# Performance work log

Measured on AMD Instinct MI355X. Metric: run time of the kernel, lower is better.

The kernel has to match this reference:

```python
import jax, jax.numpy as jnp
import numpy as np

NUM_CLASSES = 10
LAMBDA_UNCERTAINTY = 0.5
IGNORE_INDEX = 10
B, H, W = 8, 512, 512


def setup_inputs() -> dict:
    key = jax.random.key(0)
    k1, k2 = jax.random.split(key)
    logits = jax.random.normal(k1, (B, NUM_CLASSES, H, W), dtype=jnp.float32)
    targets = jax.random.randint(k2, (B, H, W), 0, 11)  # includes ignore_index=10
    return {"logits": logits, "targets": targets}


def reference(logits, targets):
    C = NUM_CLASSES
    f32 = logits.dtype

    # entropy of the predicted distribution (torch adds 1e-8 inside log)
    probs = jax.nn.softmax(logits, axis=1)                      # [B,C,H,W]
    log_probs = jnp.log(probs + 1e-8)
    entropy = -jnp.sum(probs * log_probs, axis=1)               # [B,H,W]

    valid = targets != IGNORE_INDEX                             # [B,H,W] bool
    valid_f = valid.astype(f32)
    n_valid = jnp.sum(valid_f)                                  # scalar

    # single-pass scatter-mean replacing the per-class python loop
    t_clip = jnp.clip(targets, 0, C - 1)
    t_flat = t_clip.reshape(-1)
    v_flat = valid_f.reshape(-1)
    counts = jax.ops.segment_sum(v_flat, t_flat, num_segments=C)                    # n_c per class
    ent_sum = jax.ops.segment_sum(entropy.reshape(-1) * v_flat, t_flat, num_segments=C)

    has_samples = (counts > 0) & (n_valid > 0)
    w_base = jnp.where(has_samples, (n_valid - counts) / jnp.maximum(n_valid, 1.0), 0.0)
    entropy_mean = jnp.where(counts > 0, ent_sum / jnp.maximum(counts, 1.0), 0.0)
    w_combined = w_base * (1.0 + LAMBDA_UNCERTAINTY * entropy_mean)                 # [C]

    weight_map = w_combined[t_clip] * valid_f                   # [B,H,W]

    # per-pixel cross entropy, zeroed at ignore_index (torch F.cross_entropy semantics)
    log_sm = jax.nn.log_softmax(logits, axis=1)                 # [B,C,H,W]
    ce = -jnp.take_along_axis(log_sm, t_clip[:, None], axis=1)[:, 0]  # [B,H,W]
    ce = ce * valid_f

    return jnp.sum(ce * weight_map) / (n_valid + 1e-6)
```

## Files before the change

kernel.cpp:

```cpp
#include <hip/hip_runtime.h>

#define NCLS 10
#define IGN 10
#define HW_ (512 * 512)
#define BATCH 8
#define NPIX (BATCH * HW_)
#define THREADS 256
#define PPT 2
#define CHUNK_PX (THREADS * PPT)
#define CHUNKS 4
#define BLOCK_PX (CHUNK_PX * CHUNKS)
#define NBLOCKS (NPIX / BLOCK_PX)
#define STAT_STRIDE 16
#define LAMBDA_UNC 0.5f
#define LOG2E 1.4426950408889634f
#define LN2 0.6931471805599453f

#define RSTRIDE 33
#define HISTSZ (THREADS * RSTRIDE)

typedef const __attribute__((address_space(1))) void GV;
typedef __attribute__((address_space(3))) void LV;
__device__ __forceinline__ void gload_lds16(const void* g, void* l) {
    __builtin_amdgcn_global_load_lds((GV*)g, (LV*)l, 16, 0, 0);
}

__global__ void awce_zero_stats(float* __restrict__ stats) {
    int i = threadIdx.x;
    if (i < 30 * STAT_STRIDE) stats[i] = 0.0f;
}

template <bool ATOMIC>
__global__ __launch_bounds__(THREADS) void awce_main(
    const float* __restrict__ logits,
    const int* __restrict__ targets,
    float* __restrict__ outbuf)
{
    const int tid = threadIdx.x;
    const int wave = tid >> 6;
    const int lane = tid & 63;

    __shared__ float stage[2][11][CHUNK_PX];
    __shared__ float hist[HISTSZ];
    __shared__ float red[4][32];

    const int g0 = blockIdx.x * BLOCK_PX;
    const int b = g0 >> 18;
    const int hw0 = g0 & (HW_ - 1);
    const float* lbase = logits + (size_t)b * (NCLS * (size_t)HW_);

    auto stage_chunk = [&](int k, int s) {
#pragma unroll
        for (int i = wave; i < 22; i += 4) {
            const int c = i >> 1;
            const int h = i & 1;
            const int pxo = h * 256 + (lane << 2);
            const void* gsrc;
            if (c < 10)
                gsrc = (const void*)(lbase + (size_t)c * HW_ + hw0 + k * CHUNK_PX + pxo);
            else
                gsrc = (const void*)(targets + g0 + k * CHUNK_PX + pxo);
            gload_lds16(gsrc, (void*)&stage[s][c][h * 256]);
        }
    };

    stage_chunk(0, 0);
#pragma unroll
    for (int i = 0; i < RSTRIDE; ++i) hist[tid + i * THREADS] = 0.0f;
    __syncthreads();

    float* hreg = &hist[tid * RSTRIDE];

#pragma unroll
    for (int k = 0; k < CHUNKS; ++k) {
        const int s = k & 1;
        float x[NCLS][PPT];
#pragma unroll
        for (int c = 0; c < NCLS; ++c) {
            float2 v = *reinterpret_cast<float2*>(&stage[s][c][tid * PPT]);
            x[c][0] = v.x; x[c][1] = v.y;
        }
        int2 tt = *reinterpret_cast<int2*>(&stage[s][10][tid * PPT]);
        int t2[PPT] = {tt.x, tt.y};
        __builtin_amdgcn_sched_barrier(0);
        if (k + 1 < CHUNKS) stage_chunk(k + 1, s ^ 1);
#pragma unroll
        for (int j = 0; j < PPT; ++j) {
            const int tj = t2[j];
            const int tc = (tj != IGN) ? tj : NCLS;
            float m = x[0][j];
#pragma unroll
            for (int c = 1; c < NCLS; ++c) m = fmaxf(m, x[c][j]);
            const float nm2 = -m * LOG2E;
            float sum = 0.f, dot = 0.f, xt = 0.f;
#pragma unroll
            for (int c = 0; c < NCLS; ++c) {
                const float xc = x[c][j];
                const float e = __builtin_amdgcn_exp2f(fmaf(xc, LOG2E, nm2));
                sum += e;
                dot = fmaf(e, xc, dot);
                xt = (tc == c) ? xc : xt;
            }
            const float lse = fmaf(__builtin_amdgcn_logf(sum), LN2, m);
            const float rs = __builtin_amdgcn_rcpf(sum);
            const float ent = fmaf(-dot, rs, lse);
            const float ce = lse - xt;
            float* p = hreg + 3 * tc;
            p[0] += 1.0f;
            p[1] += ent;
            p[2] += ce;
        }
        __syncthreads();
    }

    if (lane < 30) {
        const int f = (lane >= 20) ? 2 : ((lane >= 10) ? 1 : 0);
        const int c = lane - f * 10;
        const int off = 3 * c + f;
        float v = 0.f;
#pragma unroll
        for (int r = 0; r < 64; ++r) v += hist[(wave * 64 + r) * RSTRIDE + off];
        red[wave][lane] = v;
    }
    __syncthreads();

    if (tid < 30) {
        float v = red[0][tid] + red[1][tid] + red[2][tid] + red[3][tid];
        if (ATOMIC) {
            atomicAdd(&outbuf[tid * STAT_STRIDE], v);
        } else {
            outbuf[tid * NBLOCKS + blockIdx.x] = v;
        }
    }
}

__global__ __launch_bounds__(512) void awce_final_partials(
    const float* __restrict__ partials, float* __restrict__ out)
{
    __shared__ float sred[32];
    const int wave = threadIdx.x >> 6;
    const int lane = threadIdx.x & 63;
#pragma unroll
    for (int k = 0; k < 4; ++k) {
        const int c = wave + k * 8;
        if (c < 30) {
            const float* col = partials + (size_t)c * NBLOCKS;
            float s = 0.f;
#pragma unroll
            for (int i = 0; i < NBLOCKS / 64; ++i) s += col[lane + 64 * i];
#pragma unroll
            for (int o = 32; o >= 1; o >>= 1) s += __shfl_xor(s, o);
            if (lane == 0) sred[c] = s;
        }
    }
    __syncthreads();
    if (threadIdx.x == 0) {
        float cnt[NCLS], es[NCLS], cs[NCLS];
        float nv = 0.f;
#pragma unroll
        for (int c = 0; c < NCLS; ++c) {
            cnt[c] = sred[c];
            es[c]  = sred[10 + c];
            cs[c]  = sred[20 + c];
            nv += cnt[c];
        }
        float loss = 0.f;
#pragma unroll
        for (int c = 0; c < NCLS; ++c) {
            float wb = 0.f;
            if (cnt[c] > 0.f && nv > 0.f) wb = (nv - cnt[c]) / fmaxf(nv, 1.f);
            const float em = (cnt[c] > 0.f) ? es[c] / fmaxf(cnt[c], 1.f) : 0.f;
            const float wc = wb * (1.f + LAMBDA_UNC * em);
            loss = fmaf(cs[c], wc, loss);
        }
        out[0] = loss / (nv + 1e-6f);
    }
}

__global__ void awce_final_atomic(const float* __restrict__ stats, float* __restrict__ out) {
    if (threadIdx.x == 0) {
        float cnt[NCLS], es[NCLS], cs[NCLS];
        float nv = 0.f;
#pragma unroll
        for (int c = 0; c < NCLS; ++c) {
            cnt[c] = stats[c * STAT_STRIDE];
            es[c]  = stats[(10 + c) * STAT_STRIDE];
            cs[c]  = stats[(20 + c) * STAT_STRIDE];
            nv += cnt[c];
        }
        float loss = 0.f;
#pragma unroll
        for (int c = 0; c < NCLS; ++c) {
            float wb = 0.f;
            if (cnt[c] > 0.f && nv > 0.f) wb = (nv - cnt[c]) / fmaxf(nv, 1.f);
            const float em = (cnt[c] > 0.f) ? es[c] / fmaxf(cnt[c], 1.f) : 0.f;
            const float wc = wb * (1.f + LAMBDA_UNC * em);
            loss = fmaf(cs[c], wc, loss);
        }
        out[0] = loss / (nv + 1e-6f);
    }
}

extern "C" void kernel_launch(void* const* d_in, const int* in_sizes, int n_in,
                              void* d_out, int out_size, void* d_ws, size_t ws_size,
                              hipStream_t stream) {
    const float* logits = (const float*)d_in[0];
    const int* targets = (const int*)d_in[1];
    float* out = (float*)d_out;
    float* ws = (float*)d_ws;

    const size_t need = (size_t)30 * NBLOCKS * sizeof(float);
    if (ws_size >= need) {
        awce_main<false><<<NBLOCKS, THREADS, 0, stream>>>(logits, targets, ws);
        awce_final_partials<<<1, 512, 0, stream>>>(ws, out);
    } else {
        awce_zero_stats<<<1, 512, 0, stream>>>(ws);
        awce_main<true><<<NBLOCKS, THREADS, 0, stream>>>(logits, targets, ws);
        awce_final_atomic<<<1, 64, 0, stream>>>(ws, out);
    }
}
```

Measured before the change: 26.84 us.

## Replace LDS-staged double-buffered loads with direct float4 register loads

```diff
diff --git a/kernel.cpp b/kernel.cpp
--- a/kernel.cpp
+++ b/kernel.cpp
@@ -5,11 +5,9 @@
 #define HW_ (512 * 512)
 #define BATCH 8
 #define NPIX (BATCH * HW_)
-#define THREADS 256
-#define PPT 2
-#define CHUNK_PX (THREADS * PPT)
-#define CHUNKS 4
-#define BLOCK_PX (CHUNK_PX * CHUNKS)
+#define THREADS 128
+#define PPT 8
+#define BLOCK_PX (THREADS * PPT)
 #define NBLOCKS (NPIX / BLOCK_PX)
 #define STAT_STRIDE 16
 #define LAMBDA_UNC 0.5f
@@ -19,19 +17,13 @@
 #define RSTRIDE 33
 #define HISTSZ (THREADS * RSTRIDE)
 
-typedef const __attribute__((address_space(1))) void GV;
-typedef __attribute__((address_space(3))) void LV;
-__device__ __forceinline__ void gload_lds16(const void* g, void* l) {
-    __builtin_amdgcn_global_load_lds((GV*)g, (LV*)l, 16, 0, 0);
-}
-
 __global__ void awce_zero_stats(float* __restrict__ stats) {
     int i = threadIdx.x;
     if (i < 30 * STAT_STRIDE) stats[i] = 0.0f;
 }
 
 template <bool ATOMIC>
-__global__ __launch_bounds__(THREADS) void awce_main(
+__global__ __launch_bounds__(THREADS, 4) void awce_main(
     const float* __restrict__ logits,
     const int* __restrict__ targets,
     float* __restrict__ outbuf)
@@ -40,66 +32,54 @@
     const int wave = tid >> 6;
     const int lane = tid & 63;
 
-    __shared__ float stage[2][11][CHUNK_PX];
     __shared__ float hist[HISTSZ];
-    __shared__ float red[4][32];
+    __shared__ float red[2][32];
 
     const int g0 = blockIdx.x * BLOCK_PX;
     const int b = g0 >> 18;
     const int hw0 = g0 & (HW_ - 1);
-    const float* lbase = logits + (size_t)b * (NCLS * (size_t)HW_);
-
-    auto stage_chunk = [&](int k, int s) {
-#pragma unroll
-        for (int i = wave; i < 22; i += 4) {
-            const int c = i >> 1;
-            const int h = i & 1;
-            const int pxo = h * 256 + (lane << 2);
-            const void* gsrc;
-            if (c < 10)
-                gsrc = (const void*)(lbase + (size_t)c * HW_ + hw0 + k * CHUNK_PX + pxo);
-            else
-                gsrc = (const void*)(targets + g0 + k * CHUNK_PX + pxo);
-            gload_lds16(gsrc, (void*)&stage[s][c][h * 256]);
-        }
-    };
-
-    stage_chunk(0, 0);
+    const float* lbase = logits + (size_t)b * (NCLS * (size_t)HW_) + hw0;
+
+    float4 xl[2][NCLS];
+    int4 tl[2];
+#pragma unroll
+    for (int h = 0; h < 2; ++h) {
+        const int po = h * 512 + tid * 4;
+#pragma unroll
+        for (int c = 0; c < NCLS; ++c)
+            xl[h][c] = *reinterpret_cast<const float4*>(lbase + (size_t)c * HW_ + po);
+        tl[h] = *reinterpret_cast<const int4*>(targets + g0 + po);
+    }
 #pragma unroll
     for (int i = 0; i < RSTRIDE; ++i) hist[tid + i * THREADS] = 0.0f;
+    __builtin_amdgcn_sched_barrier(0);
     __syncthreads();
 
     float* hreg = &hist[tid * RSTRIDE];
 
 #pragma unroll
-    for (int k = 0; k < CHUNKS; ++k) {
-        const int s = k & 1;
-        float x[NCLS][PPT];
-#pragma unroll
-        for (int c = 0; c < NCLS; ++c) {
-            float2 v = *reinterpret_cast<float2*>(&stage[s][c][tid * PPT]);
-            x[c][0] = v.x; x[c][1] = v.y;
-        }
-        int2 tt = *reinterpret_cast<int2*>(&stage[s][10][tid * PPT]);
-        int t2[PPT] = {tt.x, tt.y};
-        __builtin_amdgcn_sched_barrier(0);
-        if (k + 1 < CHUNKS) stage_chunk(k + 1, s ^ 1);
-#pragma unroll
-        for (int j = 0; j < PPT; ++j) {
-            const int tj = t2[j];
+    for (int h = 0; h < 2; ++h) {
+        const float4* xv = xl[h];
+        const int tt[4] = {tl[h].x, tl[h].y, tl[h].z, tl[h].w};
+#pragma unroll
+        for (int j = 0; j < 4; ++j) {
+            const int tj = tt[j];
             const int tc = (tj != IGN) ? tj : NCLS;
-            float m = x[0][j];
-#pragma unroll
-            for (int c = 1; c < NCLS; ++c) m = fmaxf(m, x[c][j]);
+            float x[NCLS];
+#pragma unroll
+            for (int c = 0; c < NCLS; ++c)
+                x[c] = (j == 0) ? xv[c].x : (j == 1) ? xv[c].y : (j == 2) ? xv[c].z : xv[c].w;
+            float m = x[0];
+#pragma unroll
+            for (int c = 1; c < NCLS; ++c) m = fmaxf(m, x[c]);
             const float nm2 = -m * LOG2E;
             float sum = 0.f, dot = 0.f, xt = 0.f;
 #pragma unroll
             for (int c = 0; c < NCLS; ++c) {
-                const float xc = x[c][j];
-                const float e = __builtin_amdgcn_exp2f(fmaf(xc, LOG2E, nm2));
+                const float e = __builtin_amdgcn_exp2f(fmaf(x[c], LOG2E, nm2));
                 sum += e;
-                dot = fmaf(e, xc, dot);
-                xt = (tc == c) ? xc : xt;
+                dot = fmaf(e, x[c], dot);
+                xt = (tc == c) ? x[c] : xt;
             }
             const float lse = fmaf(__builtin_amdgcn_logf(sum), LN2, m);
             const float rs = __builtin_amdgcn_rcpf(sum);
@@ -110,8 +90,9 @@
             p[1] += ent;
             p[2] += ce;
         }
-        __syncthreads();
-    }
+    }
+
+    __syncthreads();
 
     if (lane < 30) {
         const int f = (lane >= 20) ? 2 : ((lane >= 10) ? 1 : 0);
@@ -125,7 +106,7 @@
     __syncthreads();
 
     if (tid < 30) {
-        float v = red[0][tid] + red[1][tid] + red[2][tid] + red[3][tid];
+        float v = red[0][tid] + red[1][tid];
         if (ATOMIC) {
             atomicAdd(&outbuf[tid * STAT_STRIDE], v);
         } else {
```

Result: no change. 26.95 us (+0.4%).
